# Kernel optimization log

Hardware: AMD Instinct MI355X
Metric: run time of the kernel (lower is better)

## Reference

```python
import jax, jax.numpy as jnp
import numpy as np


def setup_inputs() -> dict:
    key = jax.random.key(0)
    k1, k2 = jax.random.split(key)
    x = jax.random.normal(k1, (16, 1, 512, 512), dtype=jnp.float32)
    weight = jax.random.normal(k2, (128, 1), dtype=jnp.float32)
    return {"x": x, "weight": weight}


def reference(x, weight):
    # x: [B, C=1, H, W]; weight: [K=128, D=1] codebook
    inputs = jnp.transpose(x, (0, 2, 3, 1))          # [B, H, W, C]
    input_shape = inputs.shape
    D = weight.shape[1]
    flat = inputs.reshape(-1, D)                     # [N, D]
    # pairwise squared distances: ||z||^2 + ||e||^2 - 2 z.e^T  -> [N, K]
    dist = (jnp.sum(flat ** 2, axis=1, keepdims=True)
            + jnp.sum(weight ** 2, axis=1)
            - 2.0 * flat @ weight.T)
    idx = jnp.argmin(dist, axis=1)                   # [N]
    # one-hot @ weight == gather of codebook rows (same math, no [N,K] one-hot)
    quantized = weight[idx].reshape(input_shape)     # [B, H, W, C]
    return jnp.transpose(quantized, (0, 3, 1, 2))    # [B, C, H, W]
```

## Files before the change

kernel.cpp:

```cpp
#include <hip/hip_runtime.h>


constexpr int K     = 128;
constexpr int EPT   = 8;
constexpr int BLOCK = 256;

__global__ __launch_bounds__(BLOCK) void vq_kernel(const float* __restrict__ x,
                                                   const float* __restrict__ w,
                                                   float* __restrict__ out,
                                                   long n, int kk) {
#pragma clang fp contract(off)
    __shared__ float  wraw[K];
    __shared__ float  sv[K];
    __shared__ float2 wp[K];
    __shared__ int    si[K];

    const int t = threadIdx.x;
    if (t < K) {
        wraw[t] = (t < kk) ? w[t] : __builtin_inff();
        sv[t]   = __builtin_inff();
        wp[t]   = make_float2(__builtin_inff(), __builtin_inff());
        si[t]   = 0x7fffffff;
    }
    __syncthreads();
    if (t < kk) {
        float v = wraw[t];
        int rank = 0;
        for (int j = 0; j < kk; ++j) {
            float u = wraw[j];
            rank += (u < v) || (u == v && j < t);
        }
        float v2 = v * v;
        asm volatile("" : "+v"(v2));
        sv[rank] = v;
        wp[rank] = make_float2(v, v2);
        si[rank] = t;
    }
    __syncthreads();

    const float m1  = sv[63];
    const float m2a = sv[31],  m2b = sv[95];
    const float m3a = sv[15],  m3b = sv[47], m3c = sv[79], m3d = sv[111];

    long base = ((long)blockIdx.x * BLOCK + t) * (long)EPT;
    if (base + EPT <= n) {
        float4 a = *(const float4*)(x + base);
        float4 b = *(const float4*)(x + base + 4);
        float xs[EPT] = {a.x, a.y, a.z, a.w, b.x, b.y, b.z, b.w};
        float res[EPT];
#pragma unroll
        for (int e = 0; e < EPT; ++e) {
            float xv = xs[e];
            float x2 = xv * xv;
            asm volatile("" : "+v"(x2));
            float tx = xv + xv;

            int pos = (m1 < xv) ? 64 : 0;
            float m2 = (pos & 64) ? m2b : m2a;
            pos += (m2 < xv) ? 32 : 0;
            float m3lo = (pos & 32) ? m3b : m3a;
            float m3hi = (pos & 32) ? m3d : m3c;
            float m3   = (pos & 64) ? m3hi : m3lo;
            pos += (m3 < xv) ? 16 : 0;
#pragma unroll
            for (int step = 8; step > 0; step >>= 1)
                pos += (sv[pos + step - 1] < xv) ? step : 0;

            int s = pos - 4;
            int smax = (kk > 8 ? kk : 8) - 8;
            s = s < 0 ? 0 : (s > smax ? smax : s);

            float best = __builtin_inff();
            int bestPos = s;
            float bw = 0.0f;
#pragma unroll
            for (int c = 0; c < 8; ++c) {
                float2 p = wp[s + c];
                float sum  = x2 + p.y;
                float prod = tx * p.x;
                asm volatile("" : "+v"(prod));
                float d = sum - prod;
                if (d < best) {
                    best = d; bestPos = s + c; bw = p.x;
                } else if (d == best) {
                    if (si[s + c] < si[bestPos]) { bestPos = s + c; bw = p.x; }
                }
            }
            res[e] = bw;
        }
        *(float4*)(out + base)     = make_float4(res[0], res[1], res[2], res[3]);
        *(float4*)(out + base + 4) = make_float4(res[4], res[5], res[6], res[7]);
    } else {
        for (long i = base; i < n; ++i) {
            float xv = x[i];
            float x2 = xv * xv;
            asm volatile("" : "+v"(x2));
            float tx = xv + xv;
            float best = __builtin_inff(), bwv = 0.0f;
            int bestIdx = 0x7fffffff;
            for (int p0 = 0; p0 < kk; ++p0) {
                float2 p = wp[p0];
                float sum  = x2 + p.y;
                float prod = tx * p.x;
                asm volatile("" : "+v"(prod));
                float d = sum - prod;
                if (d < best || (d == best && si[p0] < bestIdx)) {
                    best = d; bwv = p.x; bestIdx = si[p0];
                }
            }
            out[i] = bwv;
        }
    }
}

extern "C" void kernel_launch(void* const* d_in, const int* in_sizes, int n_in,
                              void* d_out, int out_size, void* d_ws, size_t ws_size,
                              hipStream_t stream) {
    const float* x = (const float*)d_in[0];
    const float* w = (const float*)d_in[1];
    float* out     = (float*)d_out;
    long n = (long)in_sizes[0];
    int  kk = in_sizes[1] < K ? in_sizes[1] : K;

    long threads_needed = (n + EPT - 1) / EPT;
    long grid = (threads_needed + BLOCK - 1) / BLOCK;
    vq_kernel<<<(int)grid, BLOCK, 0, stream>>>(x, w, out, n, kk);
}
```

Baseline: 80.90 us.

## Use level-packed search tables and branchless candidate scan with rare tie fallback

Replaces the last four binary-search steps over the sorted codebook with small per-level shared-memory tables (Eytzinger-style), so each step indexes a compact array. The 8-candidate distance scan becomes branchless select logic that recomputes w^2 on the fly instead of reading a float2 table, and tie-breaking by original index moves to a rarely taken fallback path. The aim is fewer LDS reads, less bank traffic and less divergence, in exchange for an extra barrier and a little more ALU work per candidate.

```diff
diff --git a/kernel.cpp b/kernel.cpp
--- a/kernel.cpp
+++ b/kernel.cpp
@@ -10,16 +10,18 @@
                                                    float* __restrict__ out,
                                                    long n, int kk) {
 #pragma clang fp contract(off)
-    __shared__ float  wraw[K];
-    __shared__ float  sv[K];
-    __shared__ float2 wp[K];
-    __shared__ int    si[K];
+    __shared__ float wraw[K];
+    __shared__ float sv[K];
+    __shared__ int   si[K];
+    __shared__ float t8[8];
+    __shared__ float t4[16];
+    __shared__ float t2[32];
+    __shared__ float t1[64];
 
     const int t = threadIdx.x;
     if (t < K) {
         wraw[t] = (t < kk) ? w[t] : __builtin_inff();
         sv[t]   = __builtin_inff();
-        wp[t]   = make_float2(__builtin_inff(), __builtin_inff());
         si[t]   = 0x7fffffff;
     }
     __syncthreads();
@@ -30,17 +32,20 @@
             float u = wraw[j];
             rank += (u < v) || (u == v && j < t);
         }
-        float v2 = v * v;
-        asm volatile("" : "+v"(v2));
         sv[rank] = v;
-        wp[rank] = make_float2(v, v2);
         si[rank] = t;
     }
+    __syncthreads();
+    if (t < 64) t1[t] = sv[2 * t];
+    if (t < 32) t2[t] = sv[4 * t + 1];
+    if (t < 16) t4[t] = sv[8 * t + 3];
+    if (t < 8)  t8[t] = sv[16 * t + 7];
     __syncthreads();
 
     const float m1  = sv[63];
     const float m2a = sv[31],  m2b = sv[95];
     const float m3a = sv[15],  m3b = sv[47], m3c = sv[79], m3d = sv[111];
+    const int smax = (kk > 8 ? kk : 8) - 8;
 
     long base = ((long)blockIdx.x * BLOCK + t) * (long)EPT;
     if (base + EPT <= n) {
@@ -62,31 +67,48 @@
             float m3hi = (pos & 32) ? m3d : m3c;
             float m3   = (pos & 64) ? m3hi : m3lo;
             pos += (m3 < xv) ? 16 : 0;
-#pragma unroll
-            for (int step = 8; step > 0; step >>= 1)
-                pos += (sv[pos + step - 1] < xv) ? step : 0;
+            pos += (t8[pos >> 4] < xv) ? 8 : 0;
+            pos += (t4[pos >> 3] < xv) ? 4 : 0;
+            pos += (t2[pos >> 2] < xv) ? 2 : 0;
+            pos += (t1[pos >> 1] < xv) ? 1 : 0;
 
             int s = pos - 4;
-            int smax = (kk > 8 ? kk : 8) - 8;
             s = s < 0 ? 0 : (s > smax ? smax : s);
 
             float best = __builtin_inff();
-            int bestPos = s;
-            float bw = 0.0f;
+            float bw   = 0.0f;
+            unsigned tie = 0u;
 #pragma unroll
             for (int c = 0; c < 8; ++c) {
-                float2 p = wp[s + c];
-                float sum  = x2 + p.y;
-                float prod = tx * p.x;
+                float wv = sv[s + c];
+                float w2 = wv * wv;
+                asm volatile("" : "+v"(w2));
+                float sum  = x2 + w2;
+                float prod = tx * wv;
                 asm volatile("" : "+v"(prod));
                 float d = sum - prod;
-                if (d < best) {
-                    best = d; bestPos = s + c; bw = p.x;
-                } else if (d == best) {
-                    if (si[s + c] < si[bestPos]) { bestPos = s + c; bw = p.x; }
-                }
+                bool lt = d < best;
+                tie |= (d == best) ? 1u : 0u;
+                best = lt ? d : best;
+                bw   = lt ? wv : bw;
             }
             res[e] = bw;
+            if (__builtin_expect(tie != 0u, 0)) {
+                float bb = __builtin_inff(), bwv = 0.0f;
+                int bi = 0x7fffffff;
+                for (int c = 0; c < 8; ++c) {
+                    float wv = sv[s + c];
+                    float w2 = wv * wv;
+                    asm volatile("" : "+v"(w2));
+                    float sum  = x2 + w2;
+                    float prod = tx * wv;
+                    asm volatile("" : "+v"(prod));
+                    float d = sum - prod;
+                    int oi = si[s + c];
+                    if (d < bb || (d == bb && oi < bi)) { bb = d; bi = oi; bwv = wv; }
+                }
+                res[e] = bwv;
+            }
         }
         *(float4*)(out + base)     = make_float4(res[0], res[1], res[2], res[3]);
         *(float4*)(out + base + 4) = make_float4(res[4], res[5], res[6], res[7]);
@@ -96,17 +118,18 @@
             float x2 = xv * xv;
             asm volatile("" : "+v"(x2));
             float tx = xv + xv;
-            float best = __builtin_inff(), bwv = 0.0f;
-            int bestIdx = 0x7fffffff;
+            float bb = __builtin_inff(), bwv = 0.0f;
+            int bi = 0x7fffffff;
             for (int p0 = 0; p0 < kk; ++p0) {
-                float2 p = wp[p0];
-                float sum  = x2 + p.y;
-                float prod = tx * p.x;
+                float wv = sv[p0];
+                float w2 = wv * wv;
+                asm volatile("" : "+v"(w2));
+                float sum  = x2 + w2;
+                float prod = tx * wv;
                 asm volatile("" : "+v"(prod));
                 float d = sum - prod;
-                if (d < best || (d == best && si[p0] < bestIdx)) {
-                    best = d; bwv = p.x; bestIdx = si[p0];
-                }
+                int oi = si[p0];
+                if (d < bb || (d == bb && oi < bi)) { bb = d; bi = oi; bwv = wv; }
             }
             out[i] = bwv;
         }
```

Result: slower. 84.87 us (+4.9%).
